# Performance work log

Hardware: AMD Instinct MI355X
Metric: run time of the kernel (lower is better)

The kernel has to match this reference:

```python
import jax, jax.numpy as jnp
import numpy as np

B, S, D = 1, 2048, 1024   # batch, seq_len, dim
E, H, K = 16, 1024, 4     # n_experts, expert_hidden_dim, top_k
EPS = 1e-6


def setup_inputs() -> dict:
    key = jax.random.key(0)
    ks = jax.random.split(key, 6)
    scale_d = 1.0 / np.sqrt(D)
    scale_h = 1.0 / np.sqrt(H)
    return {
        "x": jax.random.normal(ks[0], (B, S, D), dtype=jnp.float32),
        "gate_w": jax.random.normal(ks[1], (D, E), dtype=jnp.float32) * scale_d,
        "expert_bias": jnp.zeros((E,), dtype=jnp.float32),
        # SwiGLU expert weights, stacked over experts: y = (silu(x@w1) * (x@w3)) @ w2
        "w1": jax.random.normal(ks[2], (E, D, H), dtype=jnp.float32) * scale_d,
        "w3": jax.random.normal(ks[3], (E, D, H), dtype=jnp.float32) * scale_d,
        "w2": jax.random.normal(ks[4], (E, H, D), dtype=jnp.float32) * scale_h,
    }


def _moe_forward(x, gate_w, expert_bias, w1, w3, w2):
    batch, seq_len, dim = x.shape
    x_flat = x.reshape(-1, dim)                      # [T, D]
    T = x_flat.shape[0]

    # --- SigmoidRouter ---
    logits = x_flat @ gate_w + expert_bias           # [T, E]
    scores = jax.nn.sigmoid(logits)
    scores = scores / (scores.sum(axis=-1, keepdims=True) + EPS)
    weights, indices = jax.lax.top_k(scores, K)      # [T, K] each, sorted desc (matches torch.topk)
    weights = weights / (weights.sum(axis=-1, keepdims=True) + EPS)

    # load balance loss
    one_hot = jax.nn.one_hot(indices, E, dtype=jnp.float32)   # [T, K, E]
    tokens_per_expert = one_hot.sum(axis=(0, 1)) / T          # [E]
    avg_prob = scores.mean(axis=0)                            # [E]
    lb_loss = E * jnp.sum(tokens_per_expert * avg_prob)

    # per-token combine weight for each expert: sum over top-k slots
    w_te = jnp.einsum('tk,tke->te', weights, one_hot)         # [T, E]

    # --- experts (dense over E; zero combine weight == unselected) ---
    h = jnp.einsum('td,edh->eth', x_flat, w1)                 # [E, T, H]
    g = jnp.einsum('td,edh->eth', x_flat, w3)                 # [E, T, H]
    a = jax.nn.silu(h) * g                                    # SwiGLU gate
    y = jnp.einsum('eth,ehd->etd', a, w2)                     # [E, T, D]

    out = jnp.einsum('te,etd->td', w_te, y)                   # [T, D]
    return out.reshape(batch, seq_len, dim), lb_loss


def reference(x, gate_w, expert_bias, w1, w3, w2):
    return _moe_forward(x, gate_w, expert_bias, w1, w3, w2)
```

## Files before the change

kernel.cpp:

```cpp
#include <hip/hip_runtime.h>
#include <math.h>

constexpr int T_ = 2048;
constexpr int D_ = 1024;
constexpr int E_ = 16;
constexpr int H_ = 1024;
constexpr int K_ = 4;
constexpr float EPS_ = 1e-6f;

constexpr int FMT = 16;
constexpr int NTB = 8;

constexpr size_t FWS_CNT   = 0;
constexpr size_t FWS_LISTP = 256;
constexpr size_t FWS_LISTW = FWS_LISTP + (size_t)E_ * T_ * 4;
constexpr size_t FWS_NSC   = FWS_LISTW + (size_t)E_ * T_ * 4;
constexpr size_t FWS_XHI   = FWS_NSC  + (size_t)T_ * E_ * 4;
constexpr size_t FWS_XLO   = FWS_XHI  + (size_t)T_ * D_ * 2;
constexpr size_t FWS_AHI   = FWS_XLO  + (size_t)T_ * D_ * 2;
constexpr size_t FWS_ALO   = FWS_AHI  + (size_t)T_ * K_ * H_ * 2;
constexpr size_t FWS_W1S   = FWS_ALO  + (size_t)T_ * K_ * H_ * 2;
constexpr size_t FWS_W3S   = FWS_W1S  + (size_t)E_ * D_ * H_ * 4;
constexpr size_t FWS_W2S   = FWS_W3S  + (size_t)E_ * D_ * H_ * 4;
constexpr size_t FWS_NEED  = FWS_W2S  + (size_t)E_ * H_ * D_ * 4;

using short8  = __attribute__((ext_vector_type(8))) short;
using floatx4 = __attribute__((ext_vector_type(4))) float;

#define MFMA16(a, b, c) __builtin_amdgcn_mfma_f32_16x16x32_bf16((a), (b), (c), 0, 0, 0)

__device__ __forceinline__ float silu_f(float h) {
    return h / (1.f + expf(-h));
}

__device__ __forceinline__ void gll16(const void* g, void* l) {
    __builtin_amdgcn_global_load_lds(
        (const __attribute__((address_space(1))) unsigned int*)g,
        (__attribute__((address_space(3))) unsigned int*)l, 16, 0, 0);
}

__device__ __forceinline__ void pack_split8(const float f[8], unsigned short* dh, unsigned short* dl) {
    unsigned hb[8], lb[8];
#pragma unroll
    for (int i = 0; i < 8; ++i) {
        unsigned b = __float_as_uint(f[i]);
        float hf = __uint_as_float(b & 0xFFFF0000u);
        float r = f[i] - hf;
        hb[i] = b >> 16;
        lb[i] = __float_as_uint(r) >> 16;
    }
    uint4 hv, lv;
    hv.x = hb[0] | (hb[1] << 16); hv.y = hb[2] | (hb[3] << 16);
    hv.z = hb[4] | (hb[5] << 16); hv.w = hb[6] | (hb[7] << 16);
    lv.x = lb[0] | (lb[1] << 16); lv.y = lb[2] | (lb[3] << 16);
    lv.z = lb[4] | (lb[5] << 16); lv.w = lb[6] | (lb[7] << 16);
    *reinterpret_cast<uint4*>(dh) = hv;
    *reinterpret_cast<uint4*>(dl) = lv;
}

__global__ __launch_bounds__(256) void router_kernel(
    const float* __restrict__ x, const float* __restrict__ gw,
    const float* __restrict__ bias,
    int* __restrict__ cnt, float* __restrict__ nsc,
    int* __restrict__ list_p, float* __restrict__ list_w)
{
    const int t = blockIdx.x;
    const int tid = threadIdx.x;

    float part[E_];
#pragma unroll
    for (int e = 0; e < E_; ++e) part[e] = 0.f;

    const float* xr = x + (size_t)t * D_;
    for (int it = 0; it < D_ / 256; ++it) {
        int d = it * 256 + tid;
        float xv = xr[d];
        const float4* g4 = reinterpret_cast<const float4*>(gw + (size_t)d * E_);
#pragma unroll
        for (int q = 0; q < 4; ++q) {
            float4 gv = g4[q];
            part[q * 4 + 0] += xv * gv.x;
            part[q * 4 + 1] += xv * gv.y;
            part[q * 4 + 2] += xv * gv.z;
            part[q * 4 + 3] += xv * gv.w;
        }
    }
#pragma unroll
    for (int e = 0; e < E_; ++e) {
        float v = part[e];
#pragma unroll
        for (int off = 32; off > 0; off >>= 1) v += __shfl_down(v, off);
        part[e] = v;
    }
    __shared__ float red[4 * E_];
    const int wave = tid >> 6, lane = tid & 63;
    if (lane == 0) {
#pragma unroll
        for (int e = 0; e < E_; ++e) red[wave * E_ + e] = part[e];
    }
    __syncthreads();

    __shared__ float sc[E_];
    if (tid < E_) {
        float s = red[0 * E_ + tid] + red[1 * E_ + tid] + red[2 * E_ + tid] + red[3 * E_ + tid];
        s += bias[tid];
        sc[tid] = 1.f / (1.f + expf(-s));
    }
    __syncthreads();

    if (tid == 0) {
        float sum = 0.f;
#pragma unroll
        for (int e = 0; e < E_; ++e) sum += sc[e];
        float den = sum + EPS_;
        float ns[E_];
#pragma unroll
        for (int e = 0; e < E_; ++e) {
            ns[e] = sc[e] / den;
            nsc[(size_t)t * E_ + e] = ns[e];
        }
        bool used[E_];
#pragma unroll
        for (int e = 0; e < E_; ++e) used[e] = false;
        int sel[K_]; float selw[K_]; float wsum = 0.f;
        for (int k = 0; k < K_; ++k) {
            float best = -1.f; int bi = 0;
            for (int e = 0; e < E_; ++e)
                if (!used[e] && ns[e] > best) { best = ns[e]; bi = e; }
            used[bi] = true; sel[k] = bi; selw[k] = best; wsum += best;
        }
        float wden = wsum + EPS_;
        for (int k = 0; k < K_; ++k) {
            int e = sel[k];
            int slot = atomicAdd(&cnt[e], 1);
            list_p[(size_t)e * T_ + slot] = t * K_ + k;
            list_w[(size_t)e * T_ + slot] = selw[k] / wden;
        }
    }
}

__global__ __launch_bounds__(256) void conv_w(
    const float* __restrict__ w1, const float* __restrict__ w3, const float* __restrict__ w2,
    unsigned short* __restrict__ d1, unsigned short* __restrict__ d3, unsigned short* __restrict__ d2)
{
    const int b = blockIdx.x;
    const int wsel = b >> 13;
    const int rem = b & 8191;
    const int e = rem >> 9;
    const int rem2 = rem & 511;
    const int nt = rem2 >> 5;
    const int ks = rem2 & 31;
    const int tid = threadIdx.x;

    const float* src = (wsel == 0 ? w1 : wsel == 1 ? w3 : w2)
                     + ((size_t)e * 1024 + ks * 32) * 1024 + nt * 64;
    unsigned short* dst = (wsel == 0 ? d1 : wsel == 1 ? d3 : d2)
                        + ((size_t)(e * 16 + nt) * 32 + ks) * 4096;

    __shared__ float tile[32][65];
    const int r = tid >> 3, c0 = (tid & 7) * 8;
    float4 v0 = *reinterpret_cast<const float4*>(src + (size_t)r * 1024 + c0);
    float4 v1 = *reinterpret_cast<const float4*>(src + (size_t)r * 1024 + c0 + 4);
    tile[r][c0 + 0] = v0.x; tile[r][c0 + 1] = v0.y; tile[r][c0 + 2] = v0.z; tile[r][c0 + 3] = v0.w;
    tile[r][c0 + 4] = v1.x; tile[r][c0 + 5] = v1.y; tile[r][c0 + 6] = v1.z; tile[r][c0 + 7] = v1.w;
    __syncthreads();

    const int nf = tid >> 6, kc = (tid >> 4) & 3, col = tid & 15;
    float f[8];
#pragma unroll
    for (int j = 0; j < 8; ++j) f[j] = tile[kc * 8 + j][nf * 16 + col];
    pack_split8(f, dst + tid * 8, dst + 2048 + tid * 8);
}

__global__ __launch_bounds__(256) void conv_x(
    const float* __restrict__ x, unsigned short* __restrict__ xhi, unsigned short* __restrict__ xlo)
{
    const size_t i = ((size_t)blockIdx.x * 256 + threadIdx.x) * 8;
    float4 a = *reinterpret_cast<const float4*>(x + i);
    float4 b = *reinterpret_cast<const float4*>(x + i + 4);
    float f[8] = {a.x, a.y, a.z, a.w, b.x, b.y, b.z, b.w};
    pack_split8(f, xhi + i, xlo + i);
}

__global__ __launch_bounds__(256, 2) void gemm1_fast(
    const unsigned short* __restrict__ xhi, const unsigned short* __restrict__ xlo,
    const unsigned short* __restrict__ w1s, const unsigned short* __restrict__ w3s,
    const int* __restrict__ cnt, const int* __restrict__ list_p,
    unsigned short* __restrict__ a_hi, unsigned short* __restrict__ a_lo)
{
    const int bid0 = blockIdx.x;
    const int bid  = (bid0 & 7) * 256 + (bid0 >> 3);
    const int e   = bid >> 7;
    const int rem = bid & 127;
    const int mt  = rem >> 3;
    const int ntb = rem & 7;
    const int ne  = cnt[e];
    if (mt * 128 >= ne) return;
    const int tid = threadIdx.x;

    __shared__ int ps[128];
    __shared__ int ts[128];
    __shared__ alignas(16) unsigned short Ah[4096], Al[4096];
    __shared__ alignas(16) unsigned short B1h[4096], B1l[4096];
    __shared__ alignas(16) unsigned short B3h[4096], B3l[4096];

    if (tid < 128) {
        int slot = mt * 128 + tid;
        if (slot < ne) { int p = list_p[(size_t)e * T_ + slot]; ps[tid] = p; ts[tid] = p >> 2; }
        else           { ps[tid] = -1; ts[tid] = 0; }
    }
    __syncthreads();

    const int mf0 = tid >> 6, kc0 = (tid >> 4) & 3, r16 = tid & 15;
    const unsigned short* axh0 = xhi + (size_t)ts[mf0 * 16 + r16] * D_ + kc0 * 8;
    const unsigned short* axl0 = xlo + (size_t)ts[mf0 * 16 + r16] * D_ + kc0 * 8;
    const unsigned short* axh1 = xhi + (size_t)ts[(mf0 + 4) * 16 + r16] * D_ + kc0 * 8;
    const unsigned short* axl1 = xlo + (size_t)ts[(mf0 + 4) * 16 + r16] * D_ + kc0 * 8;

    const unsigned short* b1a = w1s + ((size_t)(e * 16 + ntb * 2)     * 32) * 4096 + tid * 8;
    const unsigned short* b1b = w1s + ((size_t)(e * 16 + ntb * 2 + 1) * 32) * 4096 + tid * 8;
    const unsigned short* b3a = w3s + ((size_t)(e * 16 + ntb * 2)     * 32) * 4096 + tid * 8;
    const unsigned short* b3b = w3s + ((size_t)(e * 16 + ntb * 2 + 1) * 32) * 4096 + tid * 8;

    const int w = tid >> 6, l = tid & 63;
    const int wr = w >> 1, wc = w & 1;
    const int lo8 = l * 8;

    floatx4 acch[4][4], accg[4][4];
#pragma unroll
    for (int i = 0; i < 4; ++i)
#pragma unroll
        for (int j = 0; j < 4; ++j) { acch[i][j] = (floatx4)0.f; accg[i][j] = (floatx4)0.f; }

    for (int k0 = 0; k0 < D_; k0 += 32) {
        const int ksoff = (k0 >> 5) * 4096;
        gll16(axh0 + k0, Ah + tid * 8);
        gll16(axh1 + k0, Ah + (tid + 256) * 8);
        gll16(axl0 + k0, Al + tid * 8);
        gll16(axl1 + k0, Al + (tid + 256) * 8);
        gll16(b1a + ksoff,        B1h + tid * 8);
        gll16(b1b + ksoff,        B1h + (tid + 256) * 8);
        gll16(b1a + ksoff + 2048, B1l + tid * 8);
        gll16(b1b + ksoff + 2048, B1l + (tid + 256) * 8);
        gll16(b3a + ksoff,        B3h + tid * 8);
        gll16(b3b + ksoff,        B3h + (tid + 256) * 8);
        gll16(b3a + ksoff + 2048, B3l + tid * 8);
        gll16(b3b + ksoff + 2048, B3l + (tid + 256) * 8);
        __syncthreads();

        short8 ah[4], al[4];
#pragma unroll
        for (int mi = 0; mi < 4; ++mi) {
            int base = (wr * 4 + mi) * 512 + lo8;
            ah[mi] = *reinterpret_cast<const short8*>(Ah + base);
            al[mi] = *reinterpret_cast<const short8*>(Al + base);
        }
#pragma unroll
        for (int nj = 0; nj < 4; ++nj) {
            int bb = (wc * 4 + nj) * 512 + lo8;
            short8 b1hv = *reinterpret_cast<const short8*>(B1h + bb);
            short8 b1lv = *reinterpret_cast<const short8*>(B1l + bb);
            short8 b3hv = *reinterpret_cast<const short8*>(B3h + bb);
            short8 b3lv = *reinterpret_cast<const short8*>(B3l + bb);
#pragma unroll
            for (int mi = 0; mi < 4; ++mi) {
                acch[mi][nj] = MFMA16(ah[mi], b1hv, acch[mi][nj]);
                acch[mi][nj] = MFMA16(al[mi], b1hv, acch[mi][nj]);
                acch[mi][nj] = MFMA16(ah[mi], b1lv, acch[mi][nj]);
                accg[mi][nj] = MFMA16(ah[mi], b3hv, accg[mi][nj]);
                accg[mi][nj] = MFMA16(al[mi], b3hv, accg[mi][nj]);
                accg[mi][nj] = MFMA16(ah[mi], b3lv, accg[mi][nj]);
            }
        }
        __syncthreads();
    }

    const int g4 = (l >> 4) * 4;
#pragma unroll
    for (int mi = 0; mi < 4; ++mi) {
#pragma unroll
        for (int r = 0; r < 4; ++r) {
            int m = wr * 64 + mi * 16 + g4 + r;
            int p = ps[m];
            if (p < 0) continue;
            size_t ro = (size_t)p * H_ + ntb * 128 + wc * 64 + (l & 15);
#pragma unroll
            for (int nj = 0; nj < 4; ++nj) {
                float h = acch[mi][nj][r];
                float g = accg[mi][nj][r];
                float a = silu_f(h) * g;
                unsigned b = __float_as_uint(a);
                float rr = a - __uint_as_float(b & 0xFFFF0000u);
                a_hi[ro + nj * 16] = (unsigned short)(b >> 16);
                a_lo[ro + nj * 16] = (unsigned short)(__float_as_uint(rr) >> 16);
            }
        }
    }
}

__global__ __launch_bounds__(256, 3) void gemm2_fast(
    const unsigned short* __restrict__ a_hi, const unsigned short* __restrict__ a_lo,
    const unsigned short* __restrict__ w2s, const int* __restrict__ cnt,
    const int* __restrict__ list_p, const float* __restrict__ list_w,
    float* __restrict__ out)
{
    const int bid0 = blockIdx.x;
    const int bid  = (bid0 & 7) * 256 + (bid0 >> 3);
    const int e   = bid >> 7;
    const int rem = bid & 127;
    const int mt  = rem >> 3;
    const int ntb = rem & 7;
    const int ne  = cnt[e];
    if (mt * 128 >= ne) return;
    const int tid = threadIdx.x;

    __shared__ int   ps[128];
    __shared__ float wts[128];
    __shared__ alignas(16) unsigned short Ahs[4096], Als[4096];
    __shared__ alignas(16) unsigned short Bh[4096], Bl[4096];

    if (tid < 128) {
        int slot = mt * 128 + tid;
        if (slot < ne) {
            int p = list_p[(size_t)e * T_ + slot];
            ps[tid] = p; wts[tid] = list_w[(size_t)e * T_ + slot];
        } else { ps[tid] = -1; wts[tid] = 0.f; }
    }
    __syncthreads();

    const int mf0 = tid >> 6, kc0 = (tid >> 4) & 3, r16 = tid & 15;
    int p0 = ps[mf0 * 16 + r16];      if (p0 < 0) p0 = 0;
    int p1 = ps[mf0 * 16 + 64 + r16]; if (p1 < 0) p1 = 0;
    const unsigned short* aah0 = a_hi + (size_t)p0 * H_ + kc0 * 8;
    const unsigned short* aal0 = a_lo + (size_t)p0 * H_ + kc0 * 8;
    const unsigned short* aah1 = a_hi + (size_t)p1 * H_ + kc0 * 8;
    const unsigned short* aal1 = a_lo + (size_t)p1 * H_ + kc0 * 8;

    const unsigned short* b2a = w2s + ((size_t)(e * 16 + ntb * 2)     * 32) * 4096 + tid * 8;
    const unsigned short* b2b = w2s + ((size_t)(e * 16 + ntb * 2 + 1) * 32) * 4096 + tid * 8;

    const int w = tid >> 6, l = tid & 63;
    const int wr = w >> 1, wc = w & 1;
    const int lo8 = l * 8;

    floatx4 acc[4][4];
#pragma unroll
    for (int i = 0; i < 4; ++i)
#pragma unroll
        for (int j = 0; j < 4; ++j) acc[i][j] = (floatx4)0.f;

    for (int k0 = 0; k0 < H_; k0 += 32) {
        const int ksoff = (k0 >> 5) * 4096;
        gll16(aah0 + k0, Ahs + tid * 8);
        gll16(aah1 + k0, Ahs + (tid + 256) * 8);
        gll16(aal0 + k0, Als + tid * 8);
        gll16(aal1 + k0, Als + (tid + 256) * 8);
        gll16(b2a + ksoff,        Bh + tid * 8);
        gll16(b2b + ksoff,        Bh + (tid + 256) * 8);
        gll16(b2a + ksoff + 2048, Bl + tid * 8);
        gll16(b2b + ksoff + 2048, Bl + (tid + 256) * 8);
        __syncthreads();

        short8 ah[4], al[4];
#pragma unroll
        for (int mi = 0; mi < 4; ++mi) {
            int base = (wr * 4 + mi) * 512 + lo8;
            ah[mi] = *reinterpret_cast<const short8*>(Ahs + base);
            al[mi] = *reinterpret_cast<const short8*>(Als + base);
        }
#pragma unroll
        for (int nj = 0; nj < 4; ++nj) {
            int bb = (wc * 4 + nj) * 512 + lo8;
            short8 bhv = *reinterpret_cast<const short8*>(Bh + bb);
            short8 blv = *reinterpret_cast<const short8*>(Bl + bb);
#pragma unroll
            for (int mi = 0; mi < 4; ++mi) {
                acc[mi][nj] = MFMA16(ah[mi], bhv, acc[mi][nj]);
                acc[mi][nj] = MFMA16(al[mi], bhv, acc[mi][nj]);
                acc[mi][nj] = MFMA16(ah[mi], blv, acc[mi][nj]);
            }
        }
        __syncthreads();
    }

    const int g4 = (l >> 4) * 4;
#pragma unroll
    for (int mi = 0; mi < 4; ++mi) {
#pragma unroll
        for (int r = 0; r < 4; ++r) {
            int m = wr * 64 + mi * 16 + g4 + r;
            int p = ps[m];
            if (p < 0) continue;
            int t = p >> 2;
            float wt = wts[m];
            float* dst = out + (size_t)t * D_ + ntb * 128 + wc * 64 + (l & 15);
#pragma unroll
            for (int nj = 0; nj < 4; ++nj)
                atomicAdd(dst + nj * 16, wt * acc[mi][nj][r]);
        }
    }
}

__global__ __launch_bounds__(256) void lb_kernel(
    const float* __restrict__ nsc, const int* __restrict__ cnt, float* __restrict__ out)
{
    const int tid = threadIdx.x;
    float part[E_];
#pragma unroll
    for (int e = 0; e < E_; ++e) part[e] = 0.f;
    for (int t = tid; t < T_; t += 256) {
        const float4* r4 = reinterpret_cast<const float4*>(nsc + (size_t)t * E_);
#pragma unroll
        for (int q = 0; q < 4; ++q) {
            float4 v = r4[q];
            part[q * 4 + 0] += v.x; part[q * 4 + 1] += v.y;
            part[q * 4 + 2] += v.z; part[q * 4 + 3] += v.w;
        }
    }
#pragma unroll
    for (int e = 0; e < E_; ++e) {
        float v = part[e];
#pragma unroll
        for (int off = 32; off > 0; off >>= 1) v += __shfl_down(v, off);
        part[e] = v;
    }
    __shared__ float red[4 * E_];
    const int wave = tid >> 6, lane = tid & 63;
    if (lane == 0) {
#pragma unroll
        for (int e = 0; e < E_; ++e) red[wave * E_ + e] = part[e];
    }
    __syncthreads();
    if (tid == 0) {
        float lb = 0.f;
        for (int e = 0; e < E_; ++e) {
            float s = red[0 * E_ + e] + red[1 * E_ + e] + red[2 * E_ + e] + red[3 * E_ + e];
            lb += ((float)cnt[e] / (float)T_) * (s / (float)T_);
        }
        out[(size_t)T_ * D_] = (float)E_ * lb;
    }
}

extern "C" void kernel_launch(void* const* d_in, const int* in_sizes, int n_in,
                              void* d_out, int out_size, void* d_ws, size_t ws_size,
                              hipStream_t stream)
{
    const float* x    = (const float*)d_in[0];
    const float* gw   = (const float*)d_in[1];
    const float* bias = (const float*)d_in[2];
    const float* w1   = (const float*)d_in[3];
    const float* w3   = (const float*)d_in[4];
    const float* w2   = (const float*)d_in[5];
    float* out = (float*)d_out;
    char*  ws  = (char*)d_ws;

    int*   cnt    = (int*)  (ws + FWS_CNT);
    int*   list_p = (int*)  (ws + FWS_LISTP);
    float* list_w = (float*)(ws + FWS_LISTW);
    float* nsc    = (float*)(ws + FWS_NSC);
    unsigned short* xhi  = (unsigned short*)(ws + FWS_XHI);
    unsigned short* xlo  = (unsigned short*)(ws + FWS_XLO);
    unsigned short* a_hi = (unsigned short*)(ws + FWS_AHI);
    unsigned short* a_lo = (unsigned short*)(ws + FWS_ALO);
    unsigned short* w1s  = (unsigned short*)(ws + FWS_W1S);
    unsigned short* w3s  = (unsigned short*)(ws + FWS_W3S);
    unsigned short* w2s  = (unsigned short*)(ws + FWS_W2S);

    hipMemsetAsync(d_out, 0, (size_t)out_size * sizeof(float), stream);
    hipMemsetAsync(ws, 0, 256, stream);

    conv_w<<<3 * 8192, 256, 0, stream>>>(w1, w3, w2, w1s, w3s, w2s);
    conv_x<<<T_ * D_ / (256 * 8), 256, 0, stream>>>(x, xhi, xlo);
    router_kernel<<<T_, 256, 0, stream>>>(x, gw, bias, cnt, nsc, list_p, list_w);
    gemm1_fast<<<E_ * FMT * NTB, 256, 0, stream>>>(xhi, xlo, w1s, w3s, cnt, list_p, a_hi, a_lo);
    gemm2_fast<<<E_ * FMT * NTB, 256, 0, stream>>>(a_hi, a_lo, w2s, cnt, list_p, list_w, out);
    lb_kernel<<<1, 256, 0, stream>>>(nsc, cnt, out);
}
```

Before: 577.1 us.

## Double-buffer LDS staging and halve N-tile width in expert GEMMs

Both expert GEMM kernels now stage each K-slice into one of two LDS buffers, issuing loads for the next slice while computing on the current one, and synchronising once per iteration. The N tile per block is halved from 128 to 64 columns, which doubles the grid and halves the accumulator register footprint. The aim is to overlap global-to-LDS transfers with MFMA work and to raise block count and occupancy. In exchange, each block reloads the A tile for half as many output columns, so activation reads double, and a single barrier per iteration depends on the async load ordering being correct.

```diff
diff --git a/kernel.cpp b/kernel.cpp
--- a/kernel.cpp
+++ b/kernel.cpp
@@ -9,7 +9,7 @@
 constexpr float EPS_ = 1e-6f;
 
 constexpr int FMT = 16;
-constexpr int NTB = 8;
+constexpr int FNT = 16;
 
 constexpr size_t FWS_CNT   = 0;
 constexpr size_t FWS_LISTP = 256;
@@ -189,20 +189,20 @@
     unsigned short* __restrict__ a_hi, unsigned short* __restrict__ a_lo)
 {
     const int bid0 = blockIdx.x;
-    const int bid  = (bid0 & 7) * 256 + (bid0 >> 3);
-    const int e   = bid >> 7;
-    const int rem = bid & 127;
-    const int mt  = rem >> 3;
-    const int ntb = rem & 7;
+    const int bid  = (bid0 & 7) * 512 + (bid0 >> 3);
+    const int e   = bid >> 8;
+    const int rem = bid & 255;
+    const int mt  = rem >> 4;
+    const int nt  = rem & 15;
     const int ne  = cnt[e];
     if (mt * 128 >= ne) return;
     const int tid = threadIdx.x;
 
     __shared__ int ps[128];
     __shared__ int ts[128];
-    __shared__ alignas(16) unsigned short Ah[4096], Al[4096];
-    __shared__ alignas(16) unsigned short B1h[4096], B1l[4096];
-    __shared__ alignas(16) unsigned short B3h[4096], B3l[4096];
+    __shared__ alignas(16) unsigned short Ah[2][4096], Al[2][4096];
+    __shared__ alignas(16) unsigned short B1h[2][2048], B1l[2][2048];
+    __shared__ alignas(16) unsigned short B3h[2][2048], B3l[2][2048];
 
     if (tid < 128) {
         int slot = mt * 128 + tid;
@@ -217,51 +217,52 @@
     const unsigned short* axh1 = xhi + (size_t)ts[(mf0 + 4) * 16 + r16] * D_ + kc0 * 8;
     const unsigned short* axl1 = xlo + (size_t)ts[(mf0 + 4) * 16 + r16] * D_ + kc0 * 8;
 
-    const unsigned short* b1a = w1s + ((size_t)(e * 16 + ntb * 2)     * 32) * 4096 + tid * 8;
-    const unsigned short* b1b = w1s + ((size_t)(e * 16 + ntb * 2 + 1) * 32) * 4096 + tid * 8;
-    const unsigned short* b3a = w3s + ((size_t)(e * 16 + ntb * 2)     * 32) * 4096 + tid * 8;
-    const unsigned short* b3b = w3s + ((size_t)(e * 16 + ntb * 2 + 1) * 32) * 4096 + tid * 8;
+    const unsigned short* b1a = w1s + ((size_t)(e * 16 + nt) * 32) * 4096 + tid * 8;
+    const unsigned short* b3a = w3s + ((size_t)(e * 16 + nt) * 32) * 4096 + tid * 8;
 
     const int w = tid >> 6, l = tid & 63;
     const int wr = w >> 1, wc = w & 1;
     const int lo8 = l * 8;
 
-    floatx4 acch[4][4], accg[4][4];
+    auto STAGE = [&](int buf, int ks) {
+        const int k0 = ks * 32, ksoff = ks * 4096;
+        gll16(axh0 + k0, &Ah[buf][tid * 8]);
+        gll16(axh1 + k0, &Ah[buf][(tid + 256) * 8]);
+        gll16(axl0 + k0, &Al[buf][tid * 8]);
+        gll16(axl1 + k0, &Al[buf][(tid + 256) * 8]);
+        gll16(b1a + ksoff,        &B1h[buf][tid * 8]);
+        gll16(b1a + ksoff + 2048, &B1l[buf][tid * 8]);
+        gll16(b3a + ksoff,        &B3h[buf][tid * 8]);
+        gll16(b3a + ksoff + 2048, &B3l[buf][tid * 8]);
+    };
+
+    floatx4 acch[4][2], accg[4][2];
 #pragma unroll
     for (int i = 0; i < 4; ++i)
 #pragma unroll
-        for (int j = 0; j < 4; ++j) { acch[i][j] = (floatx4)0.f; accg[i][j] = (floatx4)0.f; }
-
-    for (int k0 = 0; k0 < D_; k0 += 32) {
-        const int ksoff = (k0 >> 5) * 4096;
-        gll16(axh0 + k0, Ah + tid * 8);
-        gll16(axh1 + k0, Ah + (tid + 256) * 8);
-        gll16(axl0 + k0, Al + tid * 8);
-        gll16(axl1 + k0, Al + (tid + 256) * 8);
-        gll16(b1a + ksoff,        B1h + tid * 8);
-        gll16(b1b + ksoff,        B1h + (tid + 256) * 8);
-        gll16(b1a + ksoff + 2048, B1l + tid * 8);
-        gll16(b1b + ksoff + 2048, B1l + (tid + 256) * 8);
-        gll16(b3a + ksoff,        B3h + tid * 8);
-        gll16(b3b + ksoff,        B3h + (tid + 256) * 8);
-        gll16(b3a + ksoff + 2048, B3l + tid * 8);
-        gll16(b3b + ksoff + 2048, B3l + (tid + 256) * 8);
-        __syncthreads();
+        for (int j = 0; j < 2; ++j) { acch[i][j] = (floatx4)0.f; accg[i][j] = (floatx4)0.f; }
+
+    STAGE(0, 0);
+    __syncthreads();
+
+    for (int ks = 0; ks < 32; ++ks) {
+        const int cur = ks & 1;
+        if (ks < 31) STAGE(cur ^ 1, ks + 1);
 
         short8 ah[4], al[4];
 #pragma unroll
         for (int mi = 0; mi < 4; ++mi) {
             int base = (wr * 4 + mi) * 512 + lo8;
-            ah[mi] = *reinterpret_cast<const short8*>(Ah + base);
-            al[mi] = *reinterpret_cast<const short8*>(Al + base);
-        }
-#pragma unroll
-        for (int nj = 0; nj < 4; ++nj) {
-            int bb = (wc * 4 + nj) * 512 + lo8;
-            short8 b1hv = *reinterpret_cast<const short8*>(B1h + bb);
-            short8 b1lv = *reinterpret_cast<const short8*>(B1l + bb);
-            short8 b3hv = *reinterpret_cast<const short8*>(B3h + bb);
-            short8 b3lv = *reinterpret_cast<const short8*>(B3l + bb);
+            ah[mi] = *reinterpret_cast<const short8*>(&Ah[cur][base]);
+            al[mi] = *reinterpret_cast<const short8*>(&Al[cur][base]);
+        }
+#pragma unroll
+        for (int nj = 0; nj < 2; ++nj) {
+            int bb = (wc * 2 + nj) * 512 + lo8;
+            short8 b1hv = *reinterpret_cast<const short8*>(&B1h[cur][bb]);
+            short8 b1lv = *reinterpret_cast<const short8*>(&B1l[cur][bb]);
+            short8 b3hv = *reinterpret_cast<const short8*>(&B3h[cur][bb]);
+            short8 b3lv = *reinterpret_cast<const short8*>(&B3l[cur][bb]);
 #pragma unroll
             for (int mi = 0; mi < 4; ++mi) {
                 acch[mi][nj] = MFMA16(ah[mi], b1hv, acch[mi][nj]);
@@ -283,9 +284,9 @@
             int m = wr * 64 + mi * 16 + g4 + r;
             int p = ps[m];
             if (p < 0) continue;
-            size_t ro = (size_t)p * H_ + ntb * 128 + wc * 64 + (l & 15);
-#pragma unroll
-            for (int nj = 0; nj < 4; ++nj) {
+            size_t ro = (size_t)p * H_ + nt * 64 + wc * 32 + (l & 15);
+#pragma unroll
+            for (int nj = 0; nj < 2; ++nj) {
                 float h = acch[mi][nj][r];
                 float g = accg[mi][nj][r];
                 float a = silu_f(h) * g;
@@ -305,19 +306,19 @@
     float* __restrict__ out)
 {
     const int bid0 = blockIdx.x;
-    const int bid  = (bid0 & 7) * 256 + (bid0 >> 3);
-    const int e   = bid >> 7;
-    const int rem = bid & 127;
-    const int mt  = rem >> 3;
-    const int ntb = rem & 7;
+    const int bid  = (bid0 & 7) * 512 + (bid0 >> 3);
+    const int e   = bid >> 8;
+    const int rem = bid & 255;
+    const int mt  = rem >> 4;
+    const int nt  = rem & 15;
     const int ne  = cnt[e];
     if (mt * 128 >= ne) return;
     const int tid = threadIdx.x;
 
     __shared__ int   ps[128];
     __shared__ float wts[128];
-    __shared__ alignas(16) unsigned short Ahs[4096], Als[4096];
-    __shared__ alignas(16) unsigned short Bh[4096], Bl[4096];
+    __shared__ alignas(16) unsigned short Ahs[2][4096], Als[2][4096];
+    __shared__ alignas(16) unsigned short Bh[2][2048], Bl[2][2048];
 
     if (tid < 128) {
         int slot = mt * 128 + tid;
@@ -329,50 +330,54 @@
     __syncthreads();
 
     const int mf0 = tid >> 6, kc0 = (tid >> 4) & 3, r16 = tid & 15;
-    int p0 = ps[mf0 * 16 + r16];      if (p0 < 0) p0 = 0;
-    int p1 = ps[mf0 * 16 + 64 + r16]; if (p1 < 0) p1 = 0;
+    int p0 = ps[mf0 * 16 + r16];       if (p0 < 0) p0 = 0;
+    int p1 = ps[(mf0 + 4) * 16 + r16]; if (p1 < 0) p1 = 0;
     const unsigned short* aah0 = a_hi + (size_t)p0 * H_ + kc0 * 8;
     const unsigned short* aal0 = a_lo + (size_t)p0 * H_ + kc0 * 8;
     const unsigned short* aah1 = a_hi + (size_t)p1 * H_ + kc0 * 8;
     const unsigned short* aal1 = a_lo + (size_t)p1 * H_ + kc0 * 8;
 
-    const unsigned short* b2a = w2s + ((size_t)(e * 16 + ntb * 2)     * 32) * 4096 + tid * 8;
-    const unsigned short* b2b = w2s + ((size_t)(e * 16 + ntb * 2 + 1) * 32) * 4096 + tid * 8;
+    const unsigned short* b2a = w2s + ((size_t)(e * 16 + nt) * 32) * 4096 + tid * 8;
 
     const int w = tid >> 6, l = tid & 63;
     const int wr = w >> 1, wc = w & 1;
     const int lo8 = l * 8;
 
-    floatx4 acc[4][4];
+    auto STAGE = [&](int buf, int ks) {
+        const int k0 = ks * 32, ksoff = ks * 4096;
+        gll16(aah0 + k0, &Ahs[buf][tid * 8]);
+        gll16(aah1 + k0, &Ahs[buf][(tid + 256) * 8]);
+        gll16(aal0 + k0, &Als[buf][tid * 8]);
+        gll16(aal1 + k0, &Als[buf][(tid + 256) * 8]);
+        gll16(b2a + ksoff,        &Bh[buf][tid * 8]);
+        gll16(b2a + ksoff + 2048, &Bl[buf][tid * 8]);
+    };
+
+    floatx4 acc[4][2];
 #pragma unroll
     for (int i = 0; i < 4; ++i)
 #pragma unroll
-        for (int j = 0; j < 4; ++j) acc[i][j] = (floatx4)0.f;
-
-    for (int k0 = 0; k0 < H_; k0 += 32) {
-        const int ksoff = (k0 >> 5) * 4096;
-        gll16(aah0 + k0, Ahs + tid * 8);
-        gll16(aah1 + k0, Ahs + (tid + 256) * 8);
-        gll16(aal0 + k0, Als + tid * 8);
-        gll16(aal1 + k0, Als + (tid + 256) * 8);
-        gll16(b2a + ksoff,        Bh + tid * 8);
-        gll16(b2b + ksoff,        Bh + (tid + 256) * 8);
-        gll16(b2a + ksoff + 2048, Bl + tid * 8);
-        gll16(b2b + ksoff + 2048, Bl + (tid + 256) * 8);
-        __syncthreads();
+        for (int j = 0; j < 2; ++j) acc[i][j] = (floatx4)0.f;
+
+    STAGE(0, 0);
+    __syncthreads();
+
+    for (int ks = 0; ks < 32; ++ks) {
+        const int cur = ks & 1;
+        if (ks < 31) STAGE(cur ^ 1, ks + 1);
 
         short8 ah[4], al[4];
 #pragma unroll
         for (int mi = 0; mi < 4; ++mi) {
             int base = (wr * 4 + mi) * 512 + lo8;
-            ah[mi] = *reinterpret_cast<const short8*>(Ahs + base);
-            al[mi] = *reinterpret_cast<const short8*>(Als + base);
-        }
-#pragma unroll
-        for (int nj = 0; nj < 4; ++nj) {
-            int bb = (wc * 4 + nj) * 512 + lo8;
-            short8 bhv = *reinterpret_cast<const short8*>(Bh + bb);
-            short8 blv = *reinterpret_cast<const short8*>(Bl + bb);
+            ah[mi] = *reinterpret_cast<const short8*>(&Ahs[cur][base]);
+            al[mi] = *reinterpret_cast<const short8*>(&Als[cur][base]);
+        }
+#pragma unroll
+        for (int nj = 0; nj < 2; ++nj) {
+            int bb = (wc * 2 + nj) * 512 + lo8;
+            short8 bhv = *reinterpret_cast<const short8*>(&Bh[cur][bb]);
+            short8 blv = *reinterpret_cast<const short8*>(&Bl[cur][bb]);
 #pragma unroll
             for (int mi = 0; mi < 4; ++mi) {
                 acc[mi][nj] = MFMA16(ah[mi], bhv, acc[mi][nj]);
@@ -393,9 +398,9 @@
             if (p < 0) continue;
             int t = p >> 2;
             float wt = wts[m];
-            float* dst = out + (size_t)t * D_ + ntb * 128 + wc * 64 + (l & 15);
-#pragma unroll
-            for (int nj = 0; nj < 4; ++nj)
+            float* dst = out + (size_t)t * D_ + nt * 64 + wc * 32 + (l & 15);
+#pragma unroll
+            for (int nj = 0; nj < 2; ++nj)
                 atomicAdd(dst + nj * 16, wt * acc[mi][nj][r]);
         }
     }
@@ -472,7 +477,7 @@
     conv_w<<<3 * 8192, 256, 0, stream>>>(w1, w3, w2, w1s, w3s, w2s);
     conv_x<<<T_ * D_ / (256 * 8), 256, 0, stream>>>(x, xhi, xlo);
     router_kernel<<<T_, 256, 0, stream>>>(x, gw, bias, cnt, nsc, list_p, list_w);
-    gemm1_fast<<<E_ * FMT * NTB, 256, 0, stream>>>(xhi, xlo, w1s, w3s, cnt, list_p, a_hi, a_lo);
-    gemm2_fast<<<E_ * FMT * NTB, 256, 0, stream>>>(a_hi, a_lo, w2s, cnt, list_p, list_w, out);
+    gemm1_fast<<<E_ * FMT * FNT, 256, 0, stream>>>(xhi, xlo, w1s, w3s, cnt, list_p, a_hi, a_lo);
+    gemm2_fast<<<E_ * FMT * FNT, 256, 0, stream>>>(a_hi, a_lo, w2s, cnt, list_p, list_w, out);
     lb_kernel<<<1, 256, 0, stream>>>(nsc, cnt, out);
 }
```

After: 668.3 us. 15.8% more time.

## Merge preprocessing kernels into one launch and shrink gemm1 tiles for occupancy

Applied to the files above, without the earlier changes.

Weight conversion, x split and the router are combined into one kernel with a block-index dispatch, and the load-balance reduction becomes an extra block of gemm2, cutting six launches down to three. gemm1 now uses 128x64 output tiles instead of 128x128, with a 4-blocks-per-CU bound and a linear block order, so it runs twice as many blocks with fewer accumulators each. The aim is lower launch overhead and higher occupancy in gemm1. In exchange, x and the B tiles are reloaded more often, and the earlier XCD-aware block swizzle is dropped from gemm1.

```diff
diff --git a/kernel.cpp b/kernel.cpp
--- a/kernel.cpp
+++ b/kernel.cpp
@@ -7,9 +7,6 @@
 constexpr int H_ = 1024;
 constexpr int K_ = 4;
 constexpr float EPS_ = 1e-6f;
-
-constexpr int FMT = 16;
-constexpr int NTB = 8;
 
 constexpr size_t FWS_CNT   = 0;
 constexpr size_t FWS_LISTP = 256;
@@ -58,136 +55,282 @@
     *reinterpret_cast<uint4*>(dl) = lv;
 }
 
-__global__ __launch_bounds__(256) void router_kernel(
-    const float* __restrict__ x, const float* __restrict__ gw,
-    const float* __restrict__ bias,
+__global__ __launch_bounds__(256) void pre_kernel(
+    const float* __restrict__ w1, const float* __restrict__ w3, const float* __restrict__ w2,
+    unsigned short* __restrict__ d1, unsigned short* __restrict__ d3, unsigned short* __restrict__ d2,
+    const float* __restrict__ x, unsigned short* __restrict__ xhi, unsigned short* __restrict__ xlo,
+    const float* __restrict__ gw, const float* __restrict__ bias,
     int* __restrict__ cnt, float* __restrict__ nsc,
     int* __restrict__ list_p, float* __restrict__ list_w)
 {
-    const int t = blockIdx.x;
+    const int b = blockIdx.x;
     const int tid = threadIdx.x;
-
-    float part[E_];
-#pragma unroll
-    for (int e = 0; e < E_; ++e) part[e] = 0.f;
-
-    const float* xr = x + (size_t)t * D_;
-    for (int it = 0; it < D_ / 256; ++it) {
-        int d = it * 256 + tid;
-        float xv = xr[d];
-        const float4* g4 = reinterpret_cast<const float4*>(gw + (size_t)d * E_);
-#pragma unroll
-        for (int q = 0; q < 4; ++q) {
-            float4 gv = g4[q];
-            part[q * 4 + 0] += xv * gv.x;
-            part[q * 4 + 1] += xv * gv.y;
-            part[q * 4 + 2] += xv * gv.z;
-            part[q * 4 + 3] += xv * gv.w;
-        }
-    }
-#pragma unroll
-    for (int e = 0; e < E_; ++e) {
-        float v = part[e];
-#pragma unroll
-        for (int off = 32; off > 0; off >>= 1) v += __shfl_down(v, off);
-        part[e] = v;
-    }
+    __shared__ float tile[32][65];
     __shared__ float red[4 * E_];
-    const int wave = tid >> 6, lane = tid & 63;
-    if (lane == 0) {
-#pragma unroll
-        for (int e = 0; e < E_; ++e) red[wave * E_ + e] = part[e];
-    }
-    __syncthreads();
-
     __shared__ float sc[E_];
-    if (tid < E_) {
-        float s = red[0 * E_ + tid] + red[1 * E_ + tid] + red[2 * E_ + tid] + red[3 * E_ + tid];
-        s += bias[tid];
-        sc[tid] = 1.f / (1.f + expf(-s));
-    }
-    __syncthreads();
-
-    if (tid == 0) {
-        float sum = 0.f;
-#pragma unroll
-        for (int e = 0; e < E_; ++e) sum += sc[e];
-        float den = sum + EPS_;
-        float ns[E_];
+
+    if (b < 24576) {
+        const int wsel = b >> 13;
+        const int rem = b & 8191;
+        const int e = rem >> 9;
+        const int rem2 = rem & 511;
+        const int nt = rem2 >> 5;
+        const int ks = rem2 & 31;
+
+        const float* src = (wsel == 0 ? w1 : wsel == 1 ? w3 : w2)
+                         + ((size_t)e * 1024 + ks * 32) * 1024 + nt * 64;
+        unsigned short* dst = (wsel == 0 ? d1 : wsel == 1 ? d3 : d2)
+                            + ((size_t)(e * 16 + nt) * 32 + ks) * 4096;
+
+        const int r = tid >> 3, c0 = (tid & 7) * 8;
+        float4 v0 = *reinterpret_cast<const float4*>(src + (size_t)r * 1024 + c0);
+        float4 v1 = *reinterpret_cast<const float4*>(src + (size_t)r * 1024 + c0 + 4);
+        tile[r][c0 + 0] = v0.x; tile[r][c0 + 1] = v0.y; tile[r][c0 + 2] = v0.z; tile[r][c0 + 3] = v0.w;
+        tile[r][c0 + 4] = v1.x; tile[r][c0 + 5] = v1.y; tile[r][c0 + 6] = v1.z; tile[r][c0 + 7] = v1.w;
+        __syncthreads();
+
+        const int nf = tid >> 6, kc = (tid >> 4) & 3, col = tid & 15;
+        float f[8];
+#pragma unroll
+        for (int j = 0; j < 8; ++j) f[j] = tile[kc * 8 + j][nf * 16 + col];
+        pack_split8(f, dst + tid * 8, dst + 2048 + tid * 8);
+
+    } else if (b < 25600) {
+        const size_t i = ((size_t)(b - 24576) * 256 + tid) * 8;
+        float4 a = *reinterpret_cast<const float4*>(x + i);
+        float4 bb = *reinterpret_cast<const float4*>(x + i + 4);
+        float f[8] = {a.x, a.y, a.z, a.w, bb.x, bb.y, bb.z, bb.w};
+        pack_split8(f, xhi + i, xlo + i);
+
+    } else {
+        const int t = b - 25600;
+        float part[E_];
+#pragma unroll
+        for (int e = 0; e < E_; ++e) part[e] = 0.f;
+
+        const float* xr = x + (size_t)t * D_;
+        for (int it = 0; it < D_ / 256; ++it) {
+            int d = it * 256 + tid;
+            float xv = xr[d];
+            const float4* g4 = reinterpret_cast<const float4*>(gw + (size_t)d * E_);
+#pragma unroll
+            for (int q = 0; q < 4; ++q) {
+                float4 gv = g4[q];
+                part[q * 4 + 0] += xv * gv.x;
+                part[q * 4 + 1] += xv * gv.y;
+                part[q * 4 + 2] += xv * gv.z;
+                part[q * 4 + 3] += xv * gv.w;
+            }
+        }
 #pragma unroll
         for (int e = 0; e < E_; ++e) {
-            ns[e] = sc[e] / den;
-            nsc[(size_t)t * E_ + e] = ns[e];
-        }
-        bool used[E_];
-#pragma unroll
-        for (int e = 0; e < E_; ++e) used[e] = false;
-        int sel[K_]; float selw[K_]; float wsum = 0.f;
-        for (int k = 0; k < K_; ++k) {
-            float best = -1.f; int bi = 0;
-            for (int e = 0; e < E_; ++e)
-                if (!used[e] && ns[e] > best) { best = ns[e]; bi = e; }
-            used[bi] = true; sel[k] = bi; selw[k] = best; wsum += best;
-        }
-        float wden = wsum + EPS_;
-        for (int k = 0; k < K_; ++k) {
-            int e = sel[k];
-            int slot = atomicAdd(&cnt[e], 1);
-            list_p[(size_t)e * T_ + slot] = t * K_ + k;
-            list_w[(size_t)e * T_ + slot] = selw[k] / wden;
-        }
-    }
-}
-
-__global__ __launch_bounds__(256) void conv_w(
-    const float* __restrict__ w1, const float* __restrict__ w3, const float* __restrict__ w2,
-    unsigned short* __restrict__ d1, unsigned short* __restrict__ d3, unsigned short* __restrict__ d2)
-{
-    const int b = blockIdx.x;
-    const int wsel = b >> 13;
-    const int rem = b & 8191;
-    const int e = rem >> 9;
-    const int rem2 = rem & 511;
-    const int nt = rem2 >> 5;
-    const int ks = rem2 & 31;
-    const int tid = threadIdx.x;
-
-    const float* src = (wsel == 0 ? w1 : wsel == 1 ? w3 : w2)
-                     + ((size_t)e * 1024 + ks * 32) * 1024 + nt * 64;
-    unsigned short* dst = (wsel == 0 ? d1 : wsel == 1 ? d3 : d2)
-                        + ((size_t)(e * 16 + nt) * 32 + ks) * 4096;
-
-    __shared__ float tile[32][65];
-    const int r = tid >> 3, c0 = (tid & 7) * 8;
-    float4 v0 = *reinterpret_cast<const float4*>(src + (size_t)r * 1024 + c0);
-    float4 v1 = *reinterpret_cast<const float4*>(src + (size_t)r * 1024 + c0 + 4);
-    tile[r][c0 + 0] = v0.x; tile[r][c0 + 1] = v0.y; tile[r][c0 + 2] = v0.z; tile[r][c0 + 3] = v0.w;
-    tile[r][c0 + 4] = v1.x; tile[r][c0 + 5] = v1.y; tile[r][c0 + 6] = v1.z; tile[r][c0 + 7] = v1.w;
-    __syncthreads();
-
-    const int nf = tid >> 6, kc = (tid >> 4) & 3, col = tid & 15;
-    float f[8];
-#pragma unroll
-    for (int j = 0; j < 8; ++j) f[j] = tile[kc * 8 + j][nf * 16 + col];
-    pack_split8(f, dst + tid * 8, dst + 2048 + tid * 8);
-}
-
-__global__ __launch_bounds__(256) void conv_x(
-    const float* __restrict__ x, unsigned short* __restrict__ xhi, unsigned short* __restrict__ xlo)
-{
-    const size_t i = ((size_t)blockIdx.x * 256 + threadIdx.x) * 8;
-    float4 a = *reinterpret_cast<const float4*>(x + i);
-    float4 b = *reinterpret_cast<const float4*>(x + i + 4);
-    float f[8] = {a.x, a.y, a.z, a.w, b.x, b.y, b.z, b.w};
-    pack_split8(f, xhi + i, xlo + i);
-}
-
-__global__ __launch_bounds__(256, 2) void gemm1_fast(
+            float v = part[e];
+#pragma unroll
+            for (int off = 32; off > 0; off >>= 1) v += __shfl_down(v, off);
+            part[e] = v;
+        }
+        const int wave = tid >> 6, lane = tid & 63;
+        if (lane == 0) {
+#pragma unroll
+            for (int e = 0; e < E_; ++e) red[wave * E_ + e] = part[e];
+        }
+        __syncthreads();
+
+        if (tid < E_) {
+            float s = red[0 * E_ + tid] + red[1 * E_ + tid] + red[2 * E_ + tid] + red[3 * E_ + tid];
+            s += bias[tid];
+            sc[tid] = 1.f / (1.f + expf(-s));
+        }
+        __syncthreads();
+
+        if (tid == 0) {
+            float sum = 0.f;
+#pragma unroll
+            for (int e = 0; e < E_; ++e) sum += sc[e];
+            float den = sum + EPS_;
+            float ns[E_];
+#pragma unroll
+            for (int e = 0; e < E_; ++e) {
+                ns[e] = sc[e] / den;
+                nsc[(size_t)t * E_ + e] = ns[e];
+            }
+            bool used[E_];
+#pragma unroll
+            for (int e = 0; e < E_; ++e) used[e] = false;
+            int sel[K_]; float selw[K_]; float wsum = 0.f;
+            for (int k = 0; k < K_; ++k) {
+                float best = -1.f; int bi = 0;
+                for (int e = 0; e < E_; ++e)
+                    if (!used[e] && ns[e] > best) { best = ns[e]; bi = e; }
+                used[bi] = true; sel[k] = bi; selw[k] = best; wsum += best;
+            }
+            float wden = wsum + EPS_;
+            for (int k = 0; k < K_; ++k) {
+                int e = sel[k];
+                int slot = atomicAdd(&cnt[e], 1);
+                list_p[(size_t)e * T_ + slot] = t * K_ + k;
+                list_w[(size_t)e * T_ + slot] = selw[k] / wden;
+            }
+        }
+    }
+}
+
+__global__ __launch_bounds__(256, 4) void gemm1_fast(
     const unsigned short* __restrict__ xhi, const unsigned short* __restrict__ xlo,
     const unsigned short* __restrict__ w1s, const unsigned short* __restrict__ w3s,
     const int* __restrict__ cnt, const int* __restrict__ list_p,
     unsigned short* __restrict__ a_hi, unsigned short* __restrict__ a_lo)
 {
+    const int bid = blockIdx.x;
+    const int e   = bid >> 8;
+    const int rem = bid & 255;
+    const int mt  = rem >> 4;
+    const int nt  = rem & 15;
+    const int ne  = cnt[e];
+    if (mt * 128 >= ne) return;
+    const int tid = threadIdx.x;
+
+    __shared__ int ps[128];
+    __shared__ int ts[128];
+    __shared__ alignas(16) unsigned short Ah[4096], Al[4096];
+    __shared__ alignas(16) unsigned short B1h[2048], B1l[2048];
+    __shared__ alignas(16) unsigned short B3h[2048], B3l[2048];
+
+    if (tid < 128) {
+        int slot = mt * 128 + tid;
+        if (slot < ne) { int p = list_p[(size_t)e * T_ + slot]; ps[tid] = p; ts[tid] = p >> 2; }
+        else           { ps[tid] = -1; ts[tid] = 0; }
+    }
+    __syncthreads();
+
+    const int mf0 = tid >> 6, kc0 = (tid >> 4) & 3, r16 = tid & 15;
+    const unsigned short* axh0 = xhi + (size_t)ts[mf0 * 16 + r16] * D_ + kc0 * 8;
+    const unsigned short* axl0 = xlo + (size_t)ts[mf0 * 16 + r16] * D_ + kc0 * 8;
+    const unsigned short* axh1 = xhi + (size_t)ts[(mf0 + 4) * 16 + r16] * D_ + kc0 * 8;
+    const unsigned short* axl1 = xlo + (size_t)ts[(mf0 + 4) * 16 + r16] * D_ + kc0 * 8;
+
+    const unsigned short* b1base = w1s + ((size_t)(e * 16 + nt) * 32) * 4096;
+    const unsigned short* b3base = w3s + ((size_t)(e * 16 + nt) * 32) * 4096;
+
+    const int w = tid >> 6, l = tid & 63;
+    const int wr = w >> 1, wc = w & 1;
+    const int lo8 = l * 8;
+
+    floatx4 acch[4][2], accg[4][2];
+#pragma unroll
+    for (int i = 0; i < 4; ++i)
+#pragma unroll
+        for (int j = 0; j < 2; ++j) { acch[i][j] = (floatx4)0.f; accg[i][j] = (floatx4)0.f; }
+
+    for (int k0 = 0; k0 < D_; k0 += 32) {
+        const unsigned short* b1 = b1base + (size_t)(k0 >> 5) * 4096;
+        const unsigned short* b3 = b3base + (size_t)(k0 >> 5) * 4096;
+        gll16(axh0 + k0, Ah + tid * 8);
+        gll16(axh1 + k0, Ah + (tid + 256) * 8);
+        gll16(axl0 + k0, Al + tid * 8);
+        gll16(axl1 + k0, Al + (tid + 256) * 8);
+        gll16(b1 + tid * 8,        B1h + tid * 8);
+        gll16(b1 + 2048 + tid * 8, B1l + tid * 8);
+        gll16(b3 + tid * 8,        B3h + tid * 8);
+        gll16(b3 + 2048 + tid * 8, B3l + tid * 8);
+        __syncthreads();
+
+        short8 ah[4], al[4];
+#pragma unroll
+        for (int mi = 0; mi < 4; ++mi) {
+            int base = (wr * 4 + mi) * 512 + lo8;
+            ah[mi] = *reinterpret_cast<const short8*>(Ah + base);
+            al[mi] = *reinterpret_cast<const short8*>(Al + base);
+        }
+#pragma unroll
+        for (int nj = 0; nj < 2; ++nj) {
+            int bb = (wc * 2 + nj) * 512 + lo8;
+            short8 b1hv = *reinterpret_cast<const short8*>(B1h + bb);
+            short8 b1lv = *reinterpret_cast<const short8*>(B1l + bb);
+            short8 b3hv = *reinterpret_cast<const short8*>(B3h + bb);
+            short8 b3lv = *reinterpret_cast<const short8*>(B3l + bb);
+#pragma unroll
+            for (int mi = 0; mi < 4; ++mi) {
+                acch[mi][nj] = MFMA16(ah[mi], b1hv, acch[mi][nj]);
+                acch[mi][nj] = MFMA16(al[mi], b1hv, acch[mi][nj]);
+                acch[mi][nj] = MFMA16(ah[mi], b1lv, acch[mi][nj]);
+                accg[mi][nj] = MFMA16(ah[mi], b3hv, accg[mi][nj]);
+                accg[mi][nj] = MFMA16(al[mi], b3hv, accg[mi][nj]);
+                accg[mi][nj] = MFMA16(ah[mi], b3lv, accg[mi][nj]);
+            }
+        }
+        __syncthreads();
+    }
+
+    const int g4 = (l >> 4) * 4;
+#pragma unroll
+    for (int mi = 0; mi < 4; ++mi) {
+#pragma unroll
+        for (int r = 0; r < 4; ++r) {
+            int m = wr * 64 + mi * 16 + g4 + r;
+            int p = ps[m];
+            if (p < 0) continue;
+            size_t ro = (size_t)p * H_ + nt * 64 + wc * 32 + (l & 15);
+#pragma unroll
+            for (int nj = 0; nj < 2; ++nj) {
+                float h = acch[mi][nj][r];
+                float g = accg[mi][nj][r];
+                float a = silu_f(h) * g;
+                unsigned b = __float_as_uint(a);
+                float rr = a - __uint_as_float(b & 0xFFFF0000u);
+                a_hi[ro + nj * 16] = (unsigned short)(b >> 16);
+                a_lo[ro + nj * 16] = (unsigned short)(__float_as_uint(rr) >> 16);
+            }
+        }
+    }
+}
+
+__global__ __launch_bounds__(256, 3) void gemm2_fast(
+    const unsigned short* __restrict__ a_hi, const unsigned short* __restrict__ a_lo,
+    const unsigned short* __restrict__ w2s, const int* __restrict__ cnt,
+    const int* __restrict__ list_p, const float* __restrict__ list_w,
+    const float* __restrict__ nsc, float* __restrict__ out)
+{
+    const int tid = threadIdx.x;
+
+    if (blockIdx.x == 2048) {
+        float part[E_];
+#pragma unroll
+        for (int e = 0; e < E_; ++e) part[e] = 0.f;
+        for (int t = tid; t < T_; t += 256) {
+            const float4* r4 = reinterpret_cast<const float4*>(nsc + (size_t)t * E_);
+#pragma unroll
+            for (int q = 0; q < 4; ++q) {
+                float4 v = r4[q];
+                part[q * 4 + 0] += v.x; part[q * 4 + 1] += v.y;
+                part[q * 4 + 2] += v.z; part[q * 4 + 3] += v.w;
+            }
+        }
+#pragma unroll
+        for (int e = 0; e < E_; ++e) {
+            float v = part[e];
+#pragma unroll
+            for (int off = 32; off > 0; off >>= 1) v += __shfl_down(v, off);
+            part[e] = v;
+        }
+        __shared__ float red[4 * E_];
+        const int wave = tid >> 6, lane = tid & 63;
+        if (lane == 0) {
+#pragma unroll
+            for (int e = 0; e < E_; ++e) red[wave * E_ + e] = part[e];
+        }
+        __syncthreads();
+        if (tid == 0) {
+            float lb = 0.f;
+            for (int e = 0; e < E_; ++e) {
+                float s = red[0 * E_ + e] + red[1 * E_ + e] + red[2 * E_ + e] + red[3 * E_ + e];
+                lb += ((float)cnt[e] / (float)T_) * (s / (float)T_);
+            }
+            out[(size_t)T_ * D_] = (float)E_ * lb;
+        }
+        return;
+    }
+
     const int bid0 = blockIdx.x;
     const int bid  = (bid0 & 7) * 256 + (bid0 >> 3);
     const int e   = bid >> 7;
@@ -196,123 +339,6 @@
     const int ntb = rem & 7;
     const int ne  = cnt[e];
     if (mt * 128 >= ne) return;
-    const int tid = threadIdx.x;
-
-    __shared__ int ps[128];
-    __shared__ int ts[128];
-    __shared__ alignas(16) unsigned short Ah[4096], Al[4096];
-    __shared__ alignas(16) unsigned short B1h[4096], B1l[4096];
-    __shared__ alignas(16) unsigned short B3h[4096], B3l[4096];
-
-    if (tid < 128) {
-        int slot = mt * 128 + tid;
-        if (slot < ne) { int p = list_p[(size_t)e * T_ + slot]; ps[tid] = p; ts[tid] = p >> 2; }
-        else           { ps[tid] = -1; ts[tid] = 0; }
-    }
-    __syncthreads();
-
-    const int mf0 = tid >> 6, kc0 = (tid >> 4) & 3, r16 = tid & 15;
-    const unsigned short* axh0 = xhi + (size_t)ts[mf0 * 16 + r16] * D_ + kc0 * 8;
-    const unsigned short* axl0 = xlo + (size_t)ts[mf0 * 16 + r16] * D_ + kc0 * 8;
-    const unsigned short* axh1 = xhi + (size_t)ts[(mf0 + 4) * 16 + r16] * D_ + kc0 * 8;
-    const unsigned short* axl1 = xlo + (size_t)ts[(mf0 + 4) * 16 + r16] * D_ + kc0 * 8;
-
-    const unsigned short* b1a = w1s + ((size_t)(e * 16 + ntb * 2)     * 32) * 4096 + tid * 8;
-    const unsigned short* b1b = w1s + ((size_t)(e * 16 + ntb * 2 + 1) * 32) * 4096 + tid * 8;
-    const unsigned short* b3a = w3s + ((size_t)(e * 16 + ntb * 2)     * 32) * 4096 + tid * 8;
-    const unsigned short* b3b = w3s + ((size_t)(e * 16 + ntb * 2 + 1) * 32) * 4096 + tid * 8;
-
-    const int w = tid >> 6, l = tid & 63;
-    const int wr = w >> 1, wc = w & 1;
-    const int lo8 = l * 8;
-
-    floatx4 acch[4][4], accg[4][4];
-#pragma unroll
-    for (int i = 0; i < 4; ++i)
-#pragma unroll
-        for (int j = 0; j < 4; ++j) { acch[i][j] = (floatx4)0.f; accg[i][j] = (floatx4)0.f; }
-
-    for (int k0 = 0; k0 < D_; k0 += 32) {
-        const int ksoff = (k0 >> 5) * 4096;
-        gll16(axh0 + k0, Ah + tid * 8);
-        gll16(axh1 + k0, Ah + (tid + 256) * 8);
-        gll16(axl0 + k0, Al + tid * 8);
-        gll16(axl1 + k0, Al + (tid + 256) * 8);
-        gll16(b1a + ksoff,        B1h + tid * 8);
-        gll16(b1b + ksoff,        B1h + (tid + 256) * 8);
-        gll16(b1a + ksoff + 2048, B1l + tid * 8);
-        gll16(b1b + ksoff + 2048, B1l + (tid + 256) * 8);
-        gll16(b3a + ksoff,        B3h + tid * 8);
-        gll16(b3b + ksoff,        B3h + (tid + 256) * 8);
-        gll16(b3a + ksoff + 2048, B3l + tid * 8);
-        gll16(b3b + ksoff + 2048, B3l + (tid + 256) * 8);
-        __syncthreads();
-
-        short8 ah[4], al[4];
-#pragma unroll
-        for (int mi = 0; mi < 4; ++mi) {
-            int base = (wr * 4 + mi) * 512 + lo8;
-            ah[mi] = *reinterpret_cast<const short8*>(Ah + base);
-            al[mi] = *reinterpret_cast<const short8*>(Al + base);
-        }
-#pragma unroll
-        for (int nj = 0; nj < 4; ++nj) {
-            int bb = (wc * 4 + nj) * 512 + lo8;
-            short8 b1hv = *reinterpret_cast<const short8*>(B1h + bb);
-            short8 b1lv = *reinterpret_cast<const short8*>(B1l + bb);
-            short8 b3hv = *reinterpret_cast<const short8*>(B3h + bb);
-            short8 b3lv = *reinterpret_cast<const short8*>(B3l + bb);
-#pragma unroll
-            for (int mi = 0; mi < 4; ++mi) {
-                acch[mi][nj] = MFMA16(ah[mi], b1hv, acch[mi][nj]);
-                acch[mi][nj] = MFMA16(al[mi], b1hv, acch[mi][nj]);
-                acch[mi][nj] = MFMA16(ah[mi], b1lv, acch[mi][nj]);
-                accg[mi][nj] = MFMA16(ah[mi], b3hv, accg[mi][nj]);
-                accg[mi][nj] = MFMA16(al[mi], b3hv, accg[mi][nj]);
-                accg[mi][nj] = MFMA16(ah[mi], b3lv, accg[mi][nj]);
-            }
-        }
-        __syncthreads();
-    }
-
-    const int g4 = (l >> 4) * 4;
-#pragma unroll
-    for (int mi = 0; mi < 4; ++mi) {
-#pragma unroll
-        for (int r = 0; r < 4; ++r) {
-            int m = wr * 64 + mi * 16 + g4 + r;
-            int p = ps[m];
-            if (p < 0) continue;
-            size_t ro = (size_t)p * H_ + ntb * 128 + wc * 64 + (l & 15);
-#pragma unroll
-            for (int nj = 0; nj < 4; ++nj) {
-                float h = acch[mi][nj][r];
-                float g = accg[mi][nj][r];
-                float a = silu_f(h) * g;
-                unsigned b = __float_as_uint(a);
-                float rr = a - __uint_as_float(b & 0xFFFF0000u);
-                a_hi[ro + nj * 16] = (unsigned short)(b >> 16);
-                a_lo[ro + nj * 16] = (unsigned short)(__float_as_uint(rr) >> 16);
-            }
-        }
-    }
-}
-
-__global__ __launch_bounds__(256, 3) void gemm2_fast(
-    const unsigned short* __restrict__ a_hi, const unsigned short* __restrict__ a_lo,
-    const unsigned short* __restrict__ w2s, const int* __restrict__ cnt,
-    const int* __restrict__ list_p, const float* __restrict__ list_w,
-    float* __restrict__ out)
-{
-    const int bid0 = blockIdx.x;
-    const int bid  = (bid0 & 7) * 256 + (bid0 >> 3);
-    const int e   = bid >> 7;
-    const int rem = bid & 127;
-    const int mt  = rem >> 3;
-    const int ntb = rem & 7;
-    const int ne  = cnt[e];
-    if (mt * 128 >= ne) return;
-    const int tid = threadIdx.x;
 
     __shared__ int   ps[128];
     __shared__ float wts[128];
@@ -398,46 +424,6 @@
             for (int nj = 0; nj < 4; ++nj)
                 atomicAdd(dst + nj * 16, wt * acc[mi][nj][r]);
         }
-    }
-}
-
-__global__ __launch_bounds__(256) void lb_kernel(
-    const float* __restrict__ nsc, const int* __restrict__ cnt, float* __restrict__ out)
-{
-    const int tid = threadIdx.x;
-    float part[E_];
-#pragma unroll
-    for (int e = 0; e < E_; ++e) part[e] = 0.f;
-    for (int t = tid; t < T_; t += 256) {
-        const float4* r4 = reinterpret_cast<const float4*>(nsc + (size_t)t * E_);
-#pragma unroll
-        for (int q = 0; q < 4; ++q) {
-            float4 v = r4[q];
-            part[q * 4 + 0] += v.x; part[q * 4 + 1] += v.y;
-            part[q * 4 + 2] += v.z; part[q * 4 + 3] += v.w;
-        }
-    }
-#pragma unroll
-    for (int e = 0; e < E_; ++e) {
-        float v = part[e];
-#pragma unroll
-        for (int off = 32; off > 0; off >>= 1) v += __shfl_down(v, off);
-        part[e] = v;
-    }
-    __shared__ float red[4 * E_];
-    const int wave = tid >> 6, lane = tid & 63;
-    if (lane == 0) {
-#pragma unroll
-        for (int e = 0; e < E_; ++e) red[wave * E_ + e] = part[e];
-    }
-    __syncthreads();
-    if (tid == 0) {
-        float lb = 0.f;
-        for (int e = 0; e < E_; ++e) {
-            float s = red[0 * E_ + e] + red[1 * E_ + e] + red[2 * E_ + e] + red[3 * E_ + e];
-            lb += ((float)cnt[e] / (float)T_) * (s / (float)T_);
-        }
-        out[(size_t)T_ * D_] = (float)E_ * lb;
     }
 }
 
@@ -469,10 +455,9 @@
     hipMemsetAsync(d_out, 0, (size_t)out_size * sizeof(float), stream);
     hipMemsetAsync(ws, 0, 256, stream);
 
-    conv_w<<<3 * 8192, 256, 0, stream>>>(w1, w3, w2, w1s, w3s, w2s);
-    conv_x<<<T_ * D_ / (256 * 8), 256, 0, stream>>>(x, xhi, xlo);
-    router_kernel<<<T_, 256, 0, stream>>>(x, gw, bias, cnt, nsc, list_p, list_w);
-    gemm1_fast<<<E_ * FMT * NTB, 256, 0, stream>>>(xhi, xlo, w1s, w3s, cnt, list_p, a_hi, a_lo);
-    gemm2_fast<<<E_ * FMT * NTB, 256, 0, stream>>>(a_hi, a_lo, w2s, cnt, list_p, list_w, out);
-    lb_kernel<<<1, 256, 0, stream>>>(nsc, cnt, out);
-}
+    pre_kernel<<<27648, 256, 0, stream>>>(w1, w3, w2, w1s, w3s, w2s,
+                                          x, xhi, xlo, gw, bias,
+                                          cnt, nsc, list_p, list_w);
+    gemm1_fast<<<4096, 256, 0, stream>>>(xhi, xlo, w1s, w3s, cnt, list_p, a_hi, a_lo);
+    gemm2_fast<<<2049, 256, 0, stream>>>(a_hi, a_lo, w2s, cnt, list_p, list_w, nsc, out);
+}
```

Result: faster. 560.2 us (-2.9%).
